# Kernel tuning notes

Measured on AMD Instinct MI355X. Metric: run time of the kernel, lower is better.

The kernel has to match this reference:

```python
import jax, jax.numpy as jnp
import numpy as np

BETA_MAX = 0.01
CD_WEIGHT = 1.0
FIDELITY_WEIGHT = 0.5
BETA = BETA_MAX  # fully annealed (step >= beta_warmup)
EPS = 1e-12


def _pairwise_dist(a, b):
    """Euclidean distance matrix. a: [B,N,3], b: [B,M,3] -> [B,N,M]."""
    a2 = jnp.sum(a * a, axis=-1)                      # [B,N]
    b2 = jnp.sum(b * b, axis=-1)                      # [B,M]
    ab = jnp.einsum('bnd,bmd->bnm', a, b)             # [B,N,M]
    sq = a2[:, :, None] + b2[:, None, :] - 2.0 * ab
    return jnp.sqrt(jnp.maximum(sq, EPS))


def chamfer_distance_l1(pred, full):
    d = _pairwise_dist(pred, full)                    # [B,N,M]
    d_pf = jnp.min(d, axis=2)                         # pred -> full, [B,N]
    d_fp = jnp.min(d, axis=1)                         # full -> pred, [B,M]
    return 0.5 * (jnp.mean(d_pf) + jnp.mean(d_fp))


def fidelity_loss(partial, pred):
    # one-directional: every partial point should have a close predicted point
    d = _pairwise_dist(partial, pred)                 # [B,P,N]
    return jnp.mean(jnp.min(d, axis=2))


def kl_divergence(mu, logvar):
    # -0.5 * E_batch[ sum_dim (1 + logvar - mu^2 - exp(logvar)) ]
    kl = -0.5 * jnp.sum(1.0 + logvar - mu * mu - jnp.exp(logvar), axis=1)
    return jnp.mean(kl)


def setup_inputs() -> dict:
    key = jax.random.key(0)
    k1, k2, k3, k4, k5 = jax.random.split(key, 5)
    B, N, P, D = 8, 8192, 2048, 512
    return {
        'pred': jax.random.normal(k1, (B, N, 3), dtype=jnp.float32),
        'full': jax.random.normal(k2, (B, N, 3), dtype=jnp.float32),
        'partial': jax.random.normal(k3, (B, P, 3), dtype=jnp.float32),
        'mu': jax.random.normal(k4, (B, D), dtype=jnp.float32),
        'logvar': jax.random.normal(k5, (B, D), dtype=jnp.float32) * 0.1,
    }


def reference(pred, full, partial, mu, logvar):
    cd = chamfer_distance_l1(pred, full)
    kl = kl_divergence(mu, logvar)
    fidel = fidelity_loss(partial, pred)
    total = CD_WEIGHT * cd + BETA * kl + FIDELITY_WEIGHT * fidel
    return (total, cd, kl, fidel)
```

## Files before the change

### kernel.cpp

```cpp
#include <hip/hip_runtime.h>
#include <math.h>

#define BATCH 8
#define NPTS  8192
#define PPTS  2048
#define DLAT  512

#define YSPLIT 16
#define CHUNK  (NPTS / YSPLIT)
#define XBLK   512

typedef __attribute__((ext_vector_type(8)))  short short8;
typedef __attribute__((ext_vector_type(16))) float floatx16;

#define SEG      (2 * BATCH * NPTS + BATCH * PPTS)
#define DIR_PF   0
#define DIR_FP   (BATCH * NPTS)
#define DIR_FID  (2 * BATCH * NPTS)
#define OFF_SEG  8

__device__ __forceinline__ unsigned short f2bf(float f) {
    unsigned int u = __float_as_uint(f);
    return (unsigned short)((u + 0x7FFFu + ((u >> 16) & 1u)) >> 16);
}
__device__ __forceinline__ float bf2f(unsigned short s) {
    return __uint_as_float(((unsigned int)s) << 16);
}

__device__ __forceinline__ float min16(floatx16 d, float prev) {
    float a0 = fminf(fminf(d[0],  d[1]),  d[2]);
    float a1 = fminf(fminf(d[3],  d[4]),  d[5]);
    float a2 = fminf(fminf(d[6],  d[7]),  d[8]);
    float a3 = fminf(fminf(d[9],  d[10]), d[11]);
    float a4 = fminf(fminf(d[12], d[13]), d[14]);
    float b0 = fminf(fminf(a0, a1), a2);
    float b1 = fminf(fminf(a3, a4), d[15]);
    return fminf(fminf(b0, b1), prev);
}

__device__ __forceinline__ void encodeY(float y0, float y1, float y2,
                                        uint4* r0, uint4* r1) {
    const unsigned short h0 = f2bf(y0), h1 = f2bf(y1), h2 = f2bf(y2);
    const unsigned short l0 = f2bf(y0 - bf2f(h0));
    const unsigned short l1 = f2bf(y1 - bf2f(h1));
    const unsigned short l2 = f2bf(y2 - bf2f(h2));
    const float yn = fmaf(y0, y0, fmaf(y1, y1, y2 * y2));
    const unsigned short nh = f2bf(yn);
    const unsigned short nl = f2bf(yn - bf2f(nh));
    r0->x = (unsigned int)h0 | ((unsigned int)h1 << 16);
    r0->y = (unsigned int)h2 | ((unsigned int)l0 << 16);
    r0->z = (unsigned int)l1 | ((unsigned int)l2 << 16);
    r0->w = (unsigned int)h0 | ((unsigned int)h1 << 16);
    r1->x = (unsigned int)h2 | ((unsigned int)nh << 16);
    r1->y = (unsigned int)nl;
    r1->z = 0u; r1->w = 0u;
}

__global__ __launch_bounds__(256, 4) void minpass_kernel(
        const float* __restrict__ pred,
        const float* __restrict__ full,
        const float* __restrict__ partial,
        float* __restrict__ wsf) {
    const int bid = blockIdx.x;
    const int ys  = bid % YSPLIT;
    const int r   = bid / YSPLIT;
    const int b   = r / 36;
    const int s   = r % 36;

    const int t = threadIdx.x;

    if (bid == 0) {
        if (t < 4) wsf[t] = 0.0f;
        if (t == 4) ((unsigned int*)wsf)[4] = 0u;
    }

    const float* xset; const float* yset; int minoff; int xbase;
    if (s < 16)      { xset = pred;    yset = full; xbase = b*NPTS + s*XBLK;
                       minoff = OFF_SEG + DIR_PF  + b*NPTS + s*XBLK; }
    else if (s < 32) { xset = full;    yset = pred; xbase = b*NPTS + (s-16)*XBLK;
                       minoff = OFF_SEG + DIR_FP  + b*NPTS + (s-16)*XBLK; }
    else             { xset = partial; yset = pred; xbase = b*PPTS + (s-32)*XBLK;
                       minoff = OFF_SEG + DIR_FID + b*PPTS + (s-32)*XBLK; }

    const int lane = t & 63;
    const int wid  = t >> 6;
    const int l31  = lane & 31;
    const int half = lane >> 5;

    __shared__ uint4 sY[2][CHUNK];

    const int xw = wid * 128;
    short8 bf0, bf1, bf2, bf3;
    float  xn0, xn1, xn2, xn3;
#pragma unroll
    for (int k = 0; k < 4; ++k) {
        const float* xp = xset + (size_t)(xbase + xw + k * 32 + l31) * 3;
        const float x0 = xp[0], x1 = xp[1], x2 = xp[2];
        const float m0 = -2.0f*x0, m1 = -2.0f*x1, m2 = -2.0f*x2;
        const unsigned short h0 = f2bf(m0), h1 = f2bf(m1), h2 = f2bf(m2);
        const unsigned short l0 = f2bf(m0 - bf2f(h0));
        const unsigned short l1 = f2bf(m1 - bf2f(h1));
        const unsigned short l2 = f2bf(m2 - bf2f(h2));
        const unsigned int one = 0x3F80u;
        uint4 r0, r1;
        r0.x = (unsigned int)h0 | ((unsigned int)h1 << 16);
        r0.y = (unsigned int)h2 | ((unsigned int)h0 << 16);
        r0.z = (unsigned int)h1 | ((unsigned int)h2 << 16);
        r0.w = (unsigned int)l0 | ((unsigned int)l1 << 16);
        r1.x = (unsigned int)l2 | (one << 16);
        r1.y = one;
        r1.z = 0u; r1.w = 0u;
        const uint4 rec = half ? r1 : r0;
        const short8 bfv = *(const short8*)&rec;
        const float  xnv = fmaf(x0, x0, fmaf(x1, x1, x2 * x2));
        if (k == 0) { bf0 = bfv; xn0 = xnv; }
        else if (k == 1) { bf1 = bfv; xn1 = xnv; }
        else if (k == 2) { bf2 = bfv; xn2 = xnv; }
        else { bf3 = bfv; xn3 = xnv; }
    }

    const float* ypts = yset + (size_t)(b * NPTS + ys * CHUNK) * 3;
#pragma unroll
    for (int i = t; i < CHUNK; i += 256) {
        const float* yp = ypts + (size_t)i * 3;
        uint4 r0, r1;
        encodeY(yp[0], yp[1], yp[2], &r0, &r1);
        sY[0][i] = r0; sY[1][i] = r1;
    }
    __syncthreads();

    const floatx16 zc = {0,0,0,0, 0,0,0,0, 0,0,0,0, 0,0,0,0};
    float cmin0 = 3.4e38f, cmin1 = 3.4e38f, cmin2 = 3.4e38f, cmin3 = 3.4e38f;

    const uint4* sYh = &sY[half][0];

#define JBODY()                                                                         \
    do {                                                                                \
        const floatx16 d0 = __builtin_amdgcn_mfma_f32_32x32x16_bf16(af, bf0, zc, 0, 0, 0); \
        const floatx16 d1 = __builtin_amdgcn_mfma_f32_32x32x16_bf16(af, bf1, zc, 0, 0, 0); \
        cmin0 = min16(d0, cmin0);                                                       \
        const floatx16 d2 = __builtin_amdgcn_mfma_f32_32x32x16_bf16(af, bf2, zc, 0, 0, 0); \
        cmin1 = min16(d1, cmin1);                                                       \
        const floatx16 d3 = __builtin_amdgcn_mfma_f32_32x32x16_bf16(af, bf3, zc, 0, 0, 0); \
        cmin2 = min16(d2, cmin2);                                                       \
        cmin3 = min16(d3, cmin3);                                                       \
    } while (0)

    short8 af = *(const short8*)&sYh[l31];
#pragma unroll 8
    for (int j = 0; j < CHUNK / 32 - 1; ++j) {
        const short8 afn = *(const short8*)&sYh[(j + 1) * 32 + l31];
        JBODY();
        af = afn;
    }
    JBODY();
#undef JBODY

    const float m0 = fminf(cmin0, __shfl_xor(cmin0, 32, 64));
    const float m1 = fminf(cmin1, __shfl_xor(cmin1, 32, 64));
    const float m2 = fminf(cmin2, __shfl_xor(cmin2, 32, 64));
    const float m3 = fminf(cmin3, __shfl_xor(cmin3, 32, 64));
    if (lane < 32) {
        unsigned int* seg = (unsigned int*)wsf;
        atomicMin(&seg[minoff + xw + l31],
                  __float_as_uint(fmaxf(m0 + xn0, 0.0f)));
        atomicMin(&seg[minoff + xw + 32 + l31],
                  __float_as_uint(fmaxf(m1 + xn1, 0.0f)));
        atomicMin(&seg[minoff + xw + 64 + l31],
                  __float_as_uint(fmaxf(m2 + xn2, 0.0f)));
        atomicMin(&seg[minoff + xw + 96 + l31],
                  __float_as_uint(fmaxf(m3 + xn3, 0.0f)));
    }
}

__device__ __forceinline__ float waveReduceSum(float v) {
#pragma unroll
    for (int o = 32; o > 0; o >>= 1) v += __shfl_down(v, o, 64);
    return v;
}

__device__ __forceinline__ float blockReduceSum(float v) {
    __shared__ float wsum[4];
    const int lane = threadIdx.x & 63;
    const int wid  = threadIdx.x >> 6;
    v = waveReduceSum(v);
    if (lane == 0) wsum[wid] = v;
    __syncthreads();
    if (wid == 0) {
        v = (lane < ((int)blockDim.x >> 6)) ? wsum[lane] : 0.0f;
        v = waveReduceSum(v);
    }
    return v;
}

#define NRED_BLOCKS 145
__global__ __launch_bounds__(256) void reduce_finalize_kernel(
        float* __restrict__ wsf,
        const float* __restrict__ mu,
        const float* __restrict__ logvar,
        float* __restrict__ out) {
    float* acc = wsf;
    unsigned int* cnt = (unsigned int*)wsf + 4;
    const int bid = blockIdx.x;
    const int t   = threadIdx.x;

    float v = 0.0f;
    int accIdx;
    if (bid < 144) {
        int base;
        if (bid < 64)       { accIdx = 0; base = DIR_PF  + bid * 1024;         }
        else if (bid < 128) { accIdx = 1; base = DIR_FP  + (bid - 64) * 1024;  }
        else                { accIdx = 2; base = DIR_FID + (bid - 128) * 1024; }
#pragma unroll
        for (int k = 0; k < 4; ++k) {
            const int i = OFF_SEG + base + k * 256 + t;
            v += sqrtf(fmaxf(wsf[i], 1e-12f));
        }
    } else {
        accIdx = 3;
#pragma unroll
        for (int k = 0; k < BATCH * DLAT / 256; ++k) {
            const int i = k * 256 + t;
            const float m = mu[i];
            const float l = logvar[i];
            v += -0.5f * (1.0f + l - m * m - expf(l));
        }
    }

    v = blockReduceSum(v);
    if (t == 0) {
        atomicAdd(&acc[accIdx], v);
        __threadfence();
        const unsigned int done = atomicAdd(cnt, 1u);
        if (done == NRED_BLOCKS - 1) {
            const float s_pf  = atomicAdd(&acc[0], 0.0f);
            const float s_fp  = atomicAdd(&acc[1], 0.0f);
            const float s_fid = atomicAdd(&acc[2], 0.0f);
            const float s_kl  = atomicAdd(&acc[3], 0.0f);
            const float cd  = 0.5f * (s_pf / (float)(BATCH * NPTS) +
                                      s_fp / (float)(BATCH * NPTS));
            const float fid = s_fid / (float)(BATCH * PPTS);
            const float kl  = s_kl / (float)BATCH;
            out[0] = cd + 0.01f * kl + 0.5f * fid;
            out[1] = cd;
            out[2] = kl;
            out[3] = fid;
        }
    }
}

extern "C" void kernel_launch(void* const* d_in, const int* in_sizes, int n_in,
                              void* d_out, int out_size, void* d_ws, size_t ws_size,
                              hipStream_t stream) {
    const float* pred    = (const float*)d_in[0];
    const float* full    = (const float*)d_in[1];
    const float* partial = (const float*)d_in[2];
    const float* mu      = (const float*)d_in[3];
    const float* logvar  = (const float*)d_in[4];
    float* out = (float*)d_out;
    float* wsf = (float*)d_ws;

    hipMemsetAsync((char*)d_ws + (size_t)OFF_SEG * sizeof(float), 0x7F,
                   (size_t)SEG * sizeof(float), stream);

    minpass_kernel<<<8 * 36 * YSPLIT, 256, 0, stream>>>(pred, full, partial, wsf);

    reduce_finalize_kernel<<<NRED_BLOCKS, 256, 0, stream>>>(wsf, mu, logvar, out);
}
```

Before: 106.1 us.

## Fold x-norm into MFMA, use integer min, replace atomics with per-split partials

The squared norm of x is encoded in the bf16 hi/lo operand slots so the MFMA output is already the full squared distance. The min reduction switches to integer compares on the float bit patterns. The global atomicMin into one buffer is replaced by plain stores into YSPLIT separate partial-min buffers, which the reduce kernel then combines, so the memset is no longer needed. This costs a larger workspace (16 segments) and 16x more reads in the reduce kernel, and the main loop is fully unrolled. Integer min is only correct for non-negative floats, and slightly negative distances from bf16 rounding may order wrongly before the clamp.

```diff
diff --git a/kernel.cpp b/kernel.cpp
--- a/kernel.cpp
+++ b/kernel.cpp
@@ -27,15 +27,20 @@
     return __uint_as_float(((unsigned int)s) << 16);
 }
 
-__device__ __forceinline__ float min16(floatx16 d, float prev) {
-    float a0 = fminf(fminf(d[0],  d[1]),  d[2]);
-    float a1 = fminf(fminf(d[3],  d[4]),  d[5]);
-    float a2 = fminf(fminf(d[6],  d[7]),  d[8]);
-    float a3 = fminf(fminf(d[9],  d[10]), d[11]);
-    float a4 = fminf(fminf(d[12], d[13]), d[14]);
-    float b0 = fminf(fminf(a0, a1), a2);
-    float b1 = fminf(fminf(a3, a4), d[15]);
-    return fminf(fminf(b0, b1), prev);
+__device__ __forceinline__ int imin2(int a, int b) { return a < b ? a : b; }
+__device__ __forceinline__ int imin3(int a, int b, int c) {
+    return imin2(imin2(a, b), c);
+}
+
+__device__ __forceinline__ int min16i(floatx16 d, int prev) {
+    const int l0 = imin3(__float_as_int(d[0]),  __float_as_int(d[1]),  __float_as_int(d[2]));
+    const int l1 = imin3(__float_as_int(d[3]),  __float_as_int(d[4]),  __float_as_int(d[5]));
+    const int l2 = imin3(__float_as_int(d[6]),  __float_as_int(d[7]),  __float_as_int(d[8]));
+    const int l3 = imin3(__float_as_int(d[9]),  __float_as_int(d[10]), __float_as_int(d[11]));
+    const int l4 = imin3(__float_as_int(d[12]), __float_as_int(d[13]), __float_as_int(d[14]));
+    const int m0 = imin3(l0, l1, l2);
+    const int m1 = imin3(l3, l4, __float_as_int(d[15]));
+    return imin3(m0, m1, prev);
 }
 
 __device__ __forceinline__ void encodeY(float y0, float y1, float y2,
@@ -47,13 +52,15 @@
     const float yn = fmaf(y0, y0, fmaf(y1, y1, y2 * y2));
     const unsigned short nh = f2bf(yn);
     const unsigned short nl = f2bf(yn - bf2f(nh));
+    const unsigned int one = 0x3F80u;
     r0->x = (unsigned int)h0 | ((unsigned int)h1 << 16);
     r0->y = (unsigned int)h2 | ((unsigned int)l0 << 16);
     r0->z = (unsigned int)l1 | ((unsigned int)l2 << 16);
     r0->w = (unsigned int)h0 | ((unsigned int)h1 << 16);
     r1->x = (unsigned int)h2 | ((unsigned int)nh << 16);
-    r1->y = (unsigned int)nl;
-    r1->z = 0u; r1->w = 0u;
+    r1->y = (unsigned int)nl | (one << 16);
+    r1->z = one;
+    r1->w = 0u;
 }
 
 __global__ __launch_bounds__(256, 4) void minpass_kernel(
@@ -76,11 +83,11 @@
 
     const float* xset; const float* yset; int minoff; int xbase;
     if (s < 16)      { xset = pred;    yset = full; xbase = b*NPTS + s*XBLK;
-                       minoff = OFF_SEG + DIR_PF  + b*NPTS + s*XBLK; }
+                       minoff = OFF_SEG + ys*SEG + DIR_PF  + b*NPTS + s*XBLK; }
     else if (s < 32) { xset = full;    yset = pred; xbase = b*NPTS + (s-16)*XBLK;
-                       minoff = OFF_SEG + DIR_FP  + b*NPTS + (s-16)*XBLK; }
+                       minoff = OFF_SEG + ys*SEG + DIR_FP  + b*NPTS + (s-16)*XBLK; }
     else             { xset = partial; yset = pred; xbase = b*PPTS + (s-32)*XBLK;
-                       minoff = OFF_SEG + DIR_FID + b*PPTS + (s-32)*XBLK; }
+                       minoff = OFF_SEG + ys*SEG + DIR_FID + b*PPTS + (s-32)*XBLK; }
 
     const int lane = t & 63;
     const int wid  = t >> 6;
@@ -91,7 +98,6 @@
 
     const int xw = wid * 128;
     short8 bf0, bf1, bf2, bf3;
-    float  xn0, xn1, xn2, xn3;
 #pragma unroll
     for (int k = 0; k < 4; ++k) {
         const float* xp = xset + (size_t)(xbase + xw + k * 32 + l31) * 3;
@@ -101,6 +107,9 @@
         const unsigned short l0 = f2bf(m0 - bf2f(h0));
         const unsigned short l1 = f2bf(m1 - bf2f(h1));
         const unsigned short l2 = f2bf(m2 - bf2f(h2));
+        const float xn = fmaf(x0, x0, fmaf(x1, x1, x2 * x2));
+        const unsigned short nh = f2bf(xn);
+        const unsigned short nl = f2bf(xn - bf2f(nh));
         const unsigned int one = 0x3F80u;
         uint4 r0, r1;
         r0.x = (unsigned int)h0 | ((unsigned int)h1 << 16);
@@ -108,15 +117,15 @@
         r0.z = (unsigned int)h1 | ((unsigned int)h2 << 16);
         r0.w = (unsigned int)l0 | ((unsigned int)l1 << 16);
         r1.x = (unsigned int)l2 | (one << 16);
-        r1.y = one;
-        r1.z = 0u; r1.w = 0u;
+        r1.y = one | ((unsigned int)nh << 16);
+        r1.z = (unsigned int)nl;
+        r1.w = 0u;
         const uint4 rec = half ? r1 : r0;
         const short8 bfv = *(const short8*)&rec;
-        const float  xnv = fmaf(x0, x0, fmaf(x1, x1, x2 * x2));
-        if (k == 0) { bf0 = bfv; xn0 = xnv; }
-        else if (k == 1) { bf1 = bfv; xn1 = xnv; }
-        else if (k == 2) { bf2 = bfv; xn2 = xnv; }
-        else { bf3 = bfv; xn3 = xnv; }
+        if (k == 0) bf0 = bfv;
+        else if (k == 1) bf1 = bfv;
+        else if (k == 2) bf2 = bfv;
+        else bf3 = bfv;
     }
 
     const float* ypts = yset + (size_t)(b * NPTS + ys * CHUNK) * 3;
@@ -130,7 +139,8 @@
     __syncthreads();
 
     const floatx16 zc = {0,0,0,0, 0,0,0,0, 0,0,0,0, 0,0,0,0};
-    float cmin0 = 3.4e38f, cmin1 = 3.4e38f, cmin2 = 3.4e38f, cmin3 = 3.4e38f;
+    int cmin0 = 0x7FFFFFFF, cmin1 = 0x7FFFFFFF,
+        cmin2 = 0x7FFFFFFF, cmin3 = 0x7FFFFFFF;
 
     const uint4* sYh = &sY[half][0];
 
@@ -138,16 +148,16 @@
     do {                                                                                \
         const floatx16 d0 = __builtin_amdgcn_mfma_f32_32x32x16_bf16(af, bf0, zc, 0, 0, 0); \
         const floatx16 d1 = __builtin_amdgcn_mfma_f32_32x32x16_bf16(af, bf1, zc, 0, 0, 0); \
-        cmin0 = min16(d0, cmin0);                                                       \
+        cmin0 = min16i(d0, cmin0);                                                      \
         const floatx16 d2 = __builtin_amdgcn_mfma_f32_32x32x16_bf16(af, bf2, zc, 0, 0, 0); \
-        cmin1 = min16(d1, cmin1);                                                       \
+        cmin1 = min16i(d1, cmin1);                                                      \
         const floatx16 d3 = __builtin_amdgcn_mfma_f32_32x32x16_bf16(af, bf3, zc, 0, 0, 0); \
-        cmin2 = min16(d2, cmin2);                                                       \
-        cmin3 = min16(d3, cmin3);                                                       \
+        cmin2 = min16i(d2, cmin2);                                                      \
+        cmin3 = min16i(d3, cmin3);                                                      \
     } while (0)
 
     short8 af = *(const short8*)&sYh[l31];
-#pragma unroll 8
+#pragma unroll
     for (int j = 0; j < CHUNK / 32 - 1; ++j) {
         const short8 afn = *(const short8*)&sYh[(j + 1) * 32 + l31];
         JBODY();
@@ -156,20 +166,15 @@
     JBODY();
 #undef JBODY
 
-    const float m0 = fminf(cmin0, __shfl_xor(cmin0, 32, 64));
-    const float m1 = fminf(cmin1, __shfl_xor(cmin1, 32, 64));
-    const float m2 = fminf(cmin2, __shfl_xor(cmin2, 32, 64));
-    const float m3 = fminf(cmin3, __shfl_xor(cmin3, 32, 64));
+    const int m0 = imin2(cmin0, __shfl_xor(cmin0, 32, 64));
+    const int m1 = imin2(cmin1, __shfl_xor(cmin1, 32, 64));
+    const int m2 = imin2(cmin2, __shfl_xor(cmin2, 32, 64));
+    const int m3 = imin2(cmin3, __shfl_xor(cmin3, 32, 64));
     if (lane < 32) {
-        unsigned int* seg = (unsigned int*)wsf;
-        atomicMin(&seg[minoff + xw + l31],
-                  __float_as_uint(fmaxf(m0 + xn0, 0.0f)));
-        atomicMin(&seg[minoff + xw + 32 + l31],
-                  __float_as_uint(fmaxf(m1 + xn1, 0.0f)));
-        atomicMin(&seg[minoff + xw + 64 + l31],
-                  __float_as_uint(fmaxf(m2 + xn2, 0.0f)));
-        atomicMin(&seg[minoff + xw + 96 + l31],
-                  __float_as_uint(fmaxf(m3 + xn3, 0.0f)));
+        wsf[minoff + xw + l31]      = fmaxf(__int_as_float(m0), 0.0f);
+        wsf[minoff + xw + 32 + l31] = fmaxf(__int_as_float(m1), 0.0f);
+        wsf[minoff + xw + 64 + l31] = fmaxf(__int_as_float(m2), 0.0f);
+        wsf[minoff + xw + 96 + l31] = fmaxf(__int_as_float(m3), 0.0f);
     }
 }
 
@@ -214,7 +219,10 @@
 #pragma unroll
         for (int k = 0; k < 4; ++k) {
             const int i = OFF_SEG + base + k * 256 + t;
-            v += sqrtf(fmaxf(wsf[i], 1e-12f));
+            float m = wsf[i];
+#pragma unroll
+            for (int sg = 1; sg < YSPLIT; ++sg) m = fminf(m, wsf[i + sg * SEG]);
+            v += sqrtf(fmaxf(m, 1e-12f));
         }
     } else {
         accIdx = 3;
@@ -260,8 +268,6 @@
     float* out = (float*)d_out;
     float* wsf = (float*)d_ws;
 
-    hipMemsetAsync((char*)d_ws + (size_t)OFF_SEG * sizeof(float), 0x7F,
-                   (size_t)SEG * sizeof(float), stream);
 
     minpass_kernel<<<8 * 36 * YSPLIT, 256, 0, stream>>>(pred, full, partial, wsf);
 
```

Measured after the change: 106.4 us. Within noise of the previous version (+0.3%).
